# Optimization experiments

Hardware: AMD Instinct MI355X
Metric: run time of the kernel (lower is better)

The kernel has to match this reference:

```python
import jax, jax.numpy as jnp
import numpy as np

B, S, D = 4, 2048, 1024
H = 16            # n_heads
HD = D // H       # head_dim = 64
F = 64            # feature_dim of linear-attention feature map


def setup_inputs() -> dict:
    key = jax.random.key(0)
    ks = jax.random.split(key, 16)
    w = lambda k, shape: jax.random.normal(k, shape, dtype=jnp.float32) * 0.02
    return {
        "x": jax.random.normal(ks[0], (B, S, D), dtype=jnp.float32),
        # flash-attention branch params (Linear stored as [in, out])
        "fq": w(ks[1], (D, D)),
        "fk": w(ks[2], (D, D)),
        "fv": w(ks[3], (D, D)),
        "fo_w": w(ks[4], (D, D)),
        "fo_b": jnp.zeros((D,), jnp.float32),
        # linear-attention branch params
        "lq": w(ks[5], (D, D)),
        "lk": w(ks[6], (D, D)),
        "lv": w(ks[7], (D, D)),
        "lo_w": w(ks[8], (D, D)),
        "lo_b": jnp.zeros((D,), jnp.float32),
        "fm_w": w(ks[9], (HD, F)),
        "fm_b": jnp.zeros((F,), jnp.float32),
        # gate
        "gate_w": w(ks[10], (D, 1)),
        "gate_b": jnp.zeros((1,), jnp.float32),
    }


def reference(x, fq, fk, fv, fo_w, fo_b, lq, lk, lv, lo_w, lo_b,
              fm_w, fm_b, gate_w, gate_b):
    b, s, d = x.shape
    # ---- flash (standard softmax) attention path ----
    q = (x @ fq).reshape(b, s, H, HD)
    k = (x @ fk).reshape(b, s, H, HD)
    v = (x @ fv).reshape(b, s, H, HD)
    scale = 1.0 / np.sqrt(HD).astype(np.float32)
    scores = jnp.einsum('bqhd,bkhd->bhqk', q, k) * scale
    attn = jax.nn.softmax(scores, axis=-1)
    flash = jnp.einsum('bhqk,bkhd->bqhd', attn, v).reshape(b, s, d)
    flash_out = flash @ fo_w + fo_b
    # ---- linear (kernelized) attention path ----
    ql = (x @ lq).reshape(b, s, H, HD)
    kl = (x @ lk).reshape(b, s, H, HD)
    vl = (x @ lv).reshape(b, s, H, HD)
    qf = jax.nn.relu(ql @ fm_w + fm_b)   # [b,s,h,f]
    kf = jax.nn.relu(kl @ fm_w + fm_b)
    kv = jnp.einsum('blhf,blhd->bhfd', kf, vl)
    lin = jnp.einsum('blhf,bhfd->blhd', qf, kv)
    k_sum = kf.sum(axis=1)                               # [b,h,f]
    norm = jnp.einsum('blhf,bhf->blh', qf, k_sum)[..., None]
    lin = lin / jnp.maximum(norm, 1e-6)
    linear_out = lin.reshape(b, s, d) @ lo_w + lo_b
    # ---- sigmoid gate blend ----
    gate = jax.nn.sigmoid(x @ gate_w + gate_b)           # [b,s,1]
    return gate * flash_out + (1.0 - gate) * linear_out
```

## Files before the change

kernel.cpp:

```cpp
#include <hip/hip_runtime.h>
#include <math.h>

typedef __attribute__((ext_vector_type(4))) float f32x4;
typedef __attribute__((ext_vector_type(16))) float f32x16;
typedef __attribute__((ext_vector_type(8))) short s16x8;
typedef __attribute__((ext_vector_type(8))) unsigned short u16x8;

constexpr int Bc = 4, Sc = 2048, Dc = 1024, Hc = 16, HDc = 64, Fc = 64;
constexpr int Rc = Bc * Sc;
constexpr size_t MAT = (size_t)Rc * Dc;
constexpr int KST = 88;
constexpr int NCH = 16;

__device__ __forceinline__ float bf2f(unsigned short u) {
    union { unsigned int i; float f; } v; v.i = ((unsigned int)u) << 16; return v.f;
}
__device__ __forceinline__ unsigned short f2bf(float f) {
    union { float f; unsigned int i; } v; v.f = f;
    unsigned int r = v.i + 0x7FFFu + ((v.i >> 16) & 1u);
    return (unsigned short)(r >> 16);
}
__device__ __forceinline__ unsigned cvtpk(float a, float b) {
    unsigned r;
    asm("v_cvt_pk_bf16_f32 %0, %1, %2" : "=v"(r) : "v"(a), "v"(b));
    return r;
}
__device__ __forceinline__ void async16(const void* g, void* l) {
    __builtin_amdgcn_global_load_lds(
        (const __attribute__((address_space(1))) unsigned int*)g,
        (__attribute__((address_space(3))) unsigned int*)l, 16, 0, 0);
}

__global__ __launch_bounds__(256) void gate_cvt(const float* __restrict__ x,
        const float* __restrict__ gw, const float* __restrict__ gb,
        float* __restrict__ G, unsigned short* __restrict__ Y) {
    const int lane = threadIdx.x & 63;
    const int wave = threadIdx.x >> 6;
    const int r = blockIdx.x * 4 + wave;
    const size_t base = (size_t)r * Dc;
    float acc = 0.f;
    #pragma unroll
    for (int i = 0; i < 4; ++i) {
        int off = (lane + 64 * i) * 4;
        float4 v = *(const float4*)(x + base + off);
        float4 w = *(const float4*)(gw + off);
        acc += v.x * w.x + v.y * w.y + v.z * w.z + v.w * w.w;
        ushort4 o;
        o.x = f2bf(v.x); o.y = f2bf(v.y); o.z = f2bf(v.z); o.w = f2bf(v.w);
        *(ushort4*)(Y + base + off) = o;
    }
    #pragma unroll
    for (int off = 32; off > 0; off >>= 1) acc += __shfl_down(acc, off, 64);
    if (lane == 0) {
        float z = acc + gb[0];
        G[r] = 1.f / (1.f + __expf(-z));
    }
}

__global__ __launch_bounds__(256) void wtrans(
        const float* W0, const float* W1, const float* W2, const float* W3,
        const float* W4, const float* W5, const float* W6, const float* W7,
        unsigned short* T0, unsigned short* T1, unsigned short* T2, unsigned short* T3,
        unsigned short* T4, unsigned short* T5, unsigned short* T6, unsigned short* T7) {
    const float* W; unsigned short* T;
    switch (blockIdx.z) {
        case 0: W = W0; T = T0; break;  case 1: W = W1; T = T1; break;
        case 2: W = W2; T = T2; break;  case 3: W = W3; T = T3; break;
        case 4: W = W4; T = T4; break;  case 5: W = W5; T = T5; break;
        case 6: W = W6; T = T6; break;  default: W = W7; T = T7; break;
    }
    __shared__ float tile[64][65];
    const int t = threadIdx.x;
    const int r0 = blockIdx.x * 64, c0 = blockIdx.y * 64;
    #pragma unroll
    for (int i = 0; i < 4; ++i) {
        int row = (t >> 4) + 16 * i, col = (t & 15) * 4;
        float4 v = *(const float4*)(W + (size_t)(r0 + row) * 1024 + c0 + col);
        tile[row][col] = v.x; tile[row][col + 1] = v.y;
        tile[row][col + 2] = v.z; tile[row][col + 3] = v.w;
    }
    __syncthreads();
    #pragma unroll
    for (int i = 0; i < 4; ++i) {
        int orow = (t >> 4) + 16 * i, ocol = (t & 15) * 4;
        ushort4 o;
        o.x = f2bf(tile[ocol][orow]);     o.y = f2bf(tile[ocol + 1][orow]);
        o.z = f2bf(tile[ocol + 2][orow]); o.w = f2bf(tile[ocol + 3][orow]);
        *(ushort4*)(T + (size_t)(c0 + orow) * 1024 + r0 + ocol) = o;
    }
}

__global__ __launch_bounds__(256) void gemm3(const unsigned short* __restrict__ A,
        const unsigned short* __restrict__ WT, unsigned short* __restrict__ C0,
        unsigned short* __restrict__ C1, unsigned short* __restrict__ C2) {
    __shared__ unsigned short As[128 * 32];
    __shared__ unsigned short Bs[128 * 32];
    const int tid = threadIdx.x, wave = tid >> 6, lane = tid & 63;
    const int brow = blockIdx.x * 128;
    const int bcolg = blockIdx.y * 128;
    unsigned short* C = (blockIdx.y < 8) ? C0 : (blockIdx.y < 16 ? C1 : C2);
    const int bcol = bcolg & 1023;
    const int wm = wave >> 1, wn = wave & 1;
    const int lr = lane & 15, g8 = (lane >> 4) * 8;
    const int srow = 32 * wave + (lane >> 2);
    const int scol = (lane & 3) * 8;
    f32x4 acc[4][4];
    #pragma unroll
    for (int m = 0; m < 4; ++m)
        #pragma unroll
        for (int n = 0; n < 4; ++n) acc[m][n] = (f32x4){0.f, 0.f, 0.f, 0.f};
    for (int k0 = 0; k0 < 1024; k0 += 32) {
        __syncthreads();
        #pragma unroll
        for (int i = 0; i < 2; ++i) {
            async16(A  + (size_t)(brow  + srow + 16 * i) * 1024 + k0 + scol, &As[(32 * wave + 16 * i) * 32]);
            async16(WT + (size_t)(bcolg + srow + 16 * i) * 1024 + k0 + scol, &Bs[(32 * wave + 16 * i) * 32]);
        }
        __syncthreads();
        s16x8 af[4], bf[4];
        #pragma unroll
        for (int m = 0; m < 4; ++m) af[m] = *(const s16x8*)&As[(64 * wm + 16 * m + lr) * 32 + g8];
        #pragma unroll
        for (int n = 0; n < 4; ++n) bf[n] = *(const s16x8*)&Bs[(64 * wn + 16 * n + lr) * 32 + g8];
        #pragma unroll
        for (int m = 0; m < 4; ++m)
            #pragma unroll
            for (int n = 0; n < 4; ++n)
                acc[m][n] = __builtin_amdgcn_mfma_f32_16x16x32_bf16(af[m], bf[n], acc[m][n], 0, 0, 0);
    }
    const int rg = (lane >> 4) * 4;
    #pragma unroll
    for (int m = 0; m < 4; ++m)
        #pragma unroll
        for (int n = 0; n < 4; ++n)
            #pragma unroll
            for (int j = 0; j < 4; ++j)
                C[(size_t)(brow + 64 * wm + 16 * m + rg + j) * 1024 + bcol + 64 * wn + 16 * n + lr] =
                    f2bf(acc[m][n][j]);
}

__global__ __launch_bounds__(256) void final_gemm(const unsigned short* __restrict__ A1,
        const unsigned short* __restrict__ WT1, const unsigned short* __restrict__ A2,
        const unsigned short* __restrict__ WT2, const float* __restrict__ b1,
        const float* __restrict__ b2, const float* __restrict__ G, float* __restrict__ OUT) {
    __shared__ unsigned short As[128 * 32];
    __shared__ unsigned short Bs[128 * 32];
    const int tid = threadIdx.x, wave = tid >> 6, lane = tid & 63;
    const int brow = blockIdx.x * 128, bcol = blockIdx.y * 128;
    const int wm = wave >> 1, wn = wave & 1;
    const int lr = lane & 15, g8 = (lane >> 4) * 8;
    const int srow = 32 * wave + (lane >> 2);
    const int scol = (lane & 3) * 8;
    f32x4 acc[4][4];
    #pragma unroll
    for (int m = 0; m < 4; ++m)
        #pragma unroll
        for (int n = 0; n < 4; ++n) acc[m][n] = (f32x4){0.f, 0.f, 0.f, 0.f};
    for (int pass = 0; pass < 2; ++pass) {
        const unsigned short* A  = pass ? A2 : A1;
        const unsigned short* WT = pass ? WT2 : WT1;
        for (int k0 = 0; k0 < 1024; k0 += 32) {
            __syncthreads();
            #pragma unroll
            for (int i = 0; i < 2; ++i) {
                async16(A  + (size_t)(brow + srow + 16 * i) * 1024 + k0 + scol, &As[(32 * wave + 16 * i) * 32]);
                async16(WT + (size_t)(bcol + srow + 16 * i) * 1024 + k0 + scol, &Bs[(32 * wave + 16 * i) * 32]);
            }
            __syncthreads();
            s16x8 af[4], bf[4];
            #pragma unroll
            for (int m = 0; m < 4; ++m) af[m] = *(const s16x8*)&As[(64 * wm + 16 * m + lr) * 32 + g8];
            #pragma unroll
            for (int n = 0; n < 4; ++n) bf[n] = *(const s16x8*)&Bs[(64 * wn + 16 * n + lr) * 32 + g8];
            #pragma unroll
            for (int m = 0; m < 4; ++m)
                #pragma unroll
                for (int n = 0; n < 4; ++n)
                    acc[m][n] = __builtin_amdgcn_mfma_f32_16x16x32_bf16(af[m], bf[n], acc[m][n], 0, 0, 0);
        }
    }
    const int rg = (lane >> 4) * 4;
    #pragma unroll
    for (int m = 0; m < 4; ++m)
        #pragma unroll
        for (int j = 0; j < 4; ++j) {
            int row = brow + 64 * wm + 16 * m + rg + j;
            float g = G[row];
            #pragma unroll
            for (int n = 0; n < 4; ++n) {
                int col = bcol + 64 * wn + 16 * n + lr;
                OUT[(size_t)row * 1024 + col] = acc[m][n][j] + g * b1[col] + (1.f - g) * b2[col];
            }
        }
}

__global__ __launch_bounds__(256) void flash_mfma(const unsigned short* __restrict__ Qg,
        const unsigned short* __restrict__ Kg, const unsigned short* __restrict__ Vg,
        const float* __restrict__ G, unsigned short* __restrict__ FA) {
    __shared__ unsigned short Ks[2][64 * KST];
    __shared__ unsigned short Vt[2][64 * KST];
    const int tid = threadIdx.x, wave = tid >> 6, lane = tid & 63;
    const int b = blockIdx.z, h = blockIdx.y, q0 = blockIdx.x * 128;
    const int lq = lane & 31, hi = lane >> 5;
    const float QSCALE = 0.125f * 1.44269504f;
    const size_t qrow = (size_t)b * Sc + q0 + wave * 32 + lq;
    const size_t qoff = qrow * Dc + h * HDc + 8 * hi;
    s16x8 aq[4];
    #pragma unroll
    for (int dc = 0; dc < 4; ++dc) {
        u16x8 raw = *(const u16x8*)(Qg + qoff + 16 * dc);
        #pragma unroll
        for (int j = 0; j < 8; ++j) aq[dc][j] = (short)f2bf(bf2f(raw[j]) * QSCALE);
    }
    f32x16 oacc[2];
    #pragma unroll
    for (int t = 0; t < 2; ++t)
        #pragma unroll
        for (int r = 0; r < 16; ++r) oacc[t][r] = 0.f;
    float l_run = 0.f;
    const int srow = tid >> 3, sc8 = (tid & 7) * 8, va = tid & 7;
    const int p0 = (srow & 3) | (((srow >> 3) & 1) << 2) | (((srow >> 2) & 1) << 3) | (srow & 0x10);
    const int pg = p0 >> 3, pin = p0 & 7;
    const size_t kvoff = (size_t)h * HDc + sc8;
    #pragma unroll
    for (int r = 0; r < 2; ++r) {
        int row = srow + 32 * r;
        size_t gg = ((size_t)b * Sc + row) * Dc + kvoff;
        u16x8 kreg = *(const u16x8*)(Kg + gg);
        u16x8 vreg = *(const u16x8*)(Vg + gg);
        *(u16x8*)&Ks[0][row * KST + sc8] = kreg;
        #pragma unroll
        for (int j = 0; j < 8; ++j)
            Vt[0][(sc8 + j) * KST + 8 * ((pg + 4 * r) ^ va) + pin] = vreg[j];
    }
    __syncthreads();
    int cur = 0;
    for (int t0 = 0; t0 < Sc; t0 += 64) {
        const bool nxt = (t0 + 64) < Sc;
        u16x8 kn0, kn1, vn0, vn1;
        if (nxt) {
            size_t gg0 = ((size_t)b * Sc + t0 + 64 + srow) * Dc + kvoff;
            kn0 = *(const u16x8*)(Kg + gg0);
            vn0 = *(const u16x8*)(Vg + gg0);
            size_t gg1 = gg0 + (size_t)32 * Dc;
            kn1 = *(const u16x8*)(Kg + gg1);
            vn1 = *(const u16x8*)(Vg + gg1);
        }
        f32x16 s2[2];
        #pragma unroll
        for (int t = 0; t < 2; ++t)
            #pragma unroll
            for (int r = 0; r < 16; ++r) s2[t][r] = 0.f;
        __builtin_amdgcn_s_setprio(1);
        #pragma unroll
        for (int kt2 = 0; kt2 < 2; ++kt2)
            #pragma unroll
            for (int dc = 0; dc < 4; ++dc) {
                s16x8 ak = *(const s16x8*)&Ks[cur][(32 * kt2 + lq) * KST + 16 * dc + 8 * hi];
                s2[kt2] = __builtin_amdgcn_mfma_f32_32x32x16_bf16(ak, aq[dc], s2[kt2], 0, 0, 0);
            }
        __builtin_amdgcn_s_setprio(0);
        float ls[4] = {0.f, 0.f, 0.f, 0.f};
        #pragma unroll
        for (int t = 0; t < 2; ++t)
            #pragma unroll
            for (int r = 0; r < 16; ++r) {
                s2[t][r] = exp2f(s2[t][r]);
                ls[r & 3] += s2[t][r];
            }
        float lsum = (ls[0] + ls[1]) + (ls[2] + ls[3]);
        lsum += __shfl_xor(lsum, 32, 64);
        l_run += lsum;
        s16x8 pf[4];
        #pragma unroll
        for (int kc = 0; kc < 4; ++kc) {
            const int t = kc >> 1, e = 8 * (kc & 1);
            union { s16x8 v; unsigned u[4]; } w;
            w.u[0] = cvtpk(s2[t][e + 0], s2[t][e + 1]);
            w.u[1] = cvtpk(s2[t][e + 2], s2[t][e + 3]);
            w.u[2] = cvtpk(s2[t][e + 4], s2[t][e + 5]);
            w.u[3] = cvtpk(s2[t][e + 6], s2[t][e + 7]);
            pf[kc] = w.v;
        }
        __builtin_amdgcn_s_setprio(1);
        #pragma unroll
        for (int dtile = 0; dtile < 2; ++dtile) {
            const int row = 32 * dtile + lq;
            const int rsw = (row >> 3) & 7;
            #pragma unroll
            for (int kc = 0; kc < 4; ++kc) {
                const int g = 4 * (kc >> 1) + 2 * (kc & 1) + hi;
                s16x8 av = *(const s16x8*)&Vt[cur][row * KST + 8 * (g ^ rsw)];
                oacc[dtile] = __builtin_amdgcn_mfma_f32_32x32x16_bf16(av, pf[kc], oacc[dtile], 0, 0, 0);
            }
        }
        __builtin_amdgcn_s_setprio(0);
        if (nxt) {
            *(u16x8*)&Ks[cur ^ 1][srow * KST + sc8] = kn0;
            *(u16x8*)&Ks[cur ^ 1][(srow + 32) * KST + sc8] = kn1;
            #pragma unroll
            for (int j = 0; j < 8; ++j) {
                Vt[cur ^ 1][(sc8 + j) * KST + 8 * (pg ^ va) + pin] = vn0[j];
                Vt[cur ^ 1][(sc8 + j) * KST + 8 * ((pg + 4) ^ va) + pin] = vn1[j];
            }
        }
        __syncthreads();
        cur ^= 1;
    }
    const float scl = G[qrow] / l_run;
    #pragma unroll
    for (int dtile = 0; dtile < 2; ++dtile)
        #pragma unroll
        for (int s = 0; s < 4; ++s) {
            ushort4 o4;
            o4.x = f2bf(oacc[dtile][4 * s + 0] * scl);
            o4.y = f2bf(oacc[dtile][4 * s + 1] * scl);
            o4.z = f2bf(oacc[dtile][4 * s + 2] * scl);
            o4.w = f2bf(oacc[dtile][4 * s + 3] * scl);
            *(ushort4*)(FA + qrow * Dc + h * HDc + 32 * dtile + 8 * s + 4 * hi) = o4;
        }
}

__global__ __launch_bounds__(256) void featmap_kernel(unsigned short* __restrict__ QL,
        unsigned short* __restrict__ KL, const float* __restrict__ fmw, const float* __restrict__ fmb) {
    __shared__ float Wf[64][68];
    __shared__ float bs[64];
    __shared__ float Xs[16][68];
    const int tid = threadIdx.x;
    for (int i = tid; i < 64 * 64 / 4; i += 256) {
        int r = i >> 4, c = (i & 15) << 2;
        *(float4*)&Wf[r][c] = *(const float4*)(fmw + r * 64 + c);
    }
    if (tid < 64) bs[tid] = fmb[tid];
    const size_t row0 = (size_t)blockIdx.x * 16;
    const int rr = tid >> 4;
    const int fg = (tid & 15) << 2;
    for (int pass = 0; pass < 2; ++pass) {
        unsigned short* X = pass ? KL : QL;
        __syncthreads();
        {
            int r = tid >> 4, c = (tid & 15) << 2;
            ushort4 xv = *(const ushort4*)(X + (row0 + r) * 64 + c);
            Xs[r][c] = bf2f(xv.x); Xs[r][c + 1] = bf2f(xv.y);
            Xs[r][c + 2] = bf2f(xv.z); Xs[r][c + 3] = bf2f(xv.w);
        }
        __syncthreads();
        float a0 = bs[fg], a1 = bs[fg + 1], a2 = bs[fg + 2], a3 = bs[fg + 3];
        #pragma unroll 8
        for (int d = 0; d < 64; ++d) {
            float xv = Xs[rr][d];
            float4 w = *(const float4*)&Wf[d][fg];
            a0 += xv * w.x; a1 += xv * w.y; a2 += xv * w.z; a3 += xv * w.w;
        }
        ushort4 ov;
        ov.x = f2bf(fmaxf(a0, 0.f)); ov.y = f2bf(fmaxf(a1, 0.f));
        ov.z = f2bf(fmaxf(a2, 0.f)); ov.w = f2bf(fmaxf(a3, 0.f));
        *(ushort4*)(X + (row0 + rr) * 64 + fg) = ov;
    }
}

__global__ __launch_bounds__(256) void kv_part(const unsigned short* __restrict__ KF,
        const unsigned short* __restrict__ VL, float* __restrict__ PART, float* __restrict__ PARTS) {
    __shared__ float Ks[32][68];
    __shared__ float Vs[32][68];
    const int tid = threadIdx.x;
    const int bh = blockIdx.x;
    const int b = bh >> 4, h = bh & 15;
    const int ch = blockIdx.y;
    const int f = tid >> 2;
    const int dg = (tid & 3) << 4;
    float acc[16] = {};
    float ksum = 0.f;
    const int lbeg = ch * (Sc / NCH), lend = lbeg + Sc / NCH;
    for (int l0 = lbeg; l0 < lend; l0 += 32) {
        __syncthreads();
        for (int i = tid; i < 32 * 64 / 4; i += 256) {
            int r = i >> 4, c = (i & 15) << 2;
            size_t gg = ((size_t)(b * Sc + l0 + r) * Hc + h) * 64 + c;
            ushort4 kk = *(const ushort4*)(KF + gg);
            ushort4 vv = *(const ushort4*)(VL + gg);
            Ks[r][c] = bf2f(kk.x); Ks[r][c + 1] = bf2f(kk.y);
            Ks[r][c + 2] = bf2f(kk.z); Ks[r][c + 3] = bf2f(kk.w);
            Vs[r][c] = bf2f(vv.x); Vs[r][c + 1] = bf2f(vv.y);
            Vs[r][c + 2] = bf2f(vv.z); Vs[r][c + 3] = bf2f(vv.w);
        }
        __syncthreads();
        #pragma unroll 4
        for (int ll = 0; ll < 32; ++ll) {
            float kf = Ks[ll][f];
            ksum += kf;
            float4 v0 = *(const float4*)&Vs[ll][dg];
            float4 v1 = *(const float4*)&Vs[ll][dg + 4];
            float4 v2 = *(const float4*)&Vs[ll][dg + 8];
            float4 v3 = *(const float4*)&Vs[ll][dg + 12];
            acc[0] += kf * v0.x; acc[1] += kf * v0.y; acc[2]  += kf * v0.z; acc[3]  += kf * v0.w;
            acc[4] += kf * v1.x; acc[5] += kf * v1.y; acc[6]  += kf * v1.z; acc[7]  += kf * v1.w;
            acc[8] += kf * v2.x; acc[9] += kf * v2.y; acc[10] += kf * v2.z; acc[11] += kf * v2.w;
            acc[12] += kf * v3.x; acc[13] += kf * v3.y; acc[14] += kf * v3.z; acc[15] += kf * v3.w;
        }
    }
    size_t o = (((size_t)ch * 64 + bh) * 64 + f) * 64 + dg;
    *(float4*)(PART + o)      = make_float4(acc[0], acc[1], acc[2], acc[3]);
    *(float4*)(PART + o + 4)  = make_float4(acc[4], acc[5], acc[6], acc[7]);
    *(float4*)(PART + o + 8)  = make_float4(acc[8], acc[9], acc[10], acc[11]);
    *(float4*)(PART + o + 12) = make_float4(acc[12], acc[13], acc[14], acc[15]);
    if ((tid & 3) == 0) PARTS[((size_t)ch * 64 + bh) * 64 + f] = ksum;
}

__global__ __launch_bounds__(256) void kv_reduce(const float* __restrict__ PART,
        float* __restrict__ KV) {
    size_t i = (size_t)blockIdx.x * 256 + threadIdx.x;
    float s = 0.f;
    #pragma unroll
    for (int ch = 0; ch < NCH; ++ch) s += PART[(size_t)ch * 262144 + i];
    KV[i] = s;
}
__global__ __launch_bounds__(256) void ks_reduce(const float* __restrict__ PARTS,
        float* __restrict__ KS) {
    int i = blockIdx.x * 256 + threadIdx.x;
    float s = 0.f;
    #pragma unroll
    for (int ch = 0; ch < NCH; ++ch) s += PARTS[ch * 4096 + i];
    KS[i] = s;
}

__global__ __launch_bounds__(256) void lin_kernel(const unsigned short* __restrict__ QF,
        const float* __restrict__ KV, const float* __restrict__ KSUM,
        const float* __restrict__ G, unsigned short* __restrict__ LA) {
    __shared__ float Qs[4][68];
    __shared__ float Ss[4][68];
    const int tid = threadIdx.x;
    const size_t i0 = (size_t)blockIdx.x * 4;
    {
        int r = tid >> 6, c = tid & 63;
        size_t i = i0 + r;
        int bh = (int)(i / ((size_t)Sc * Hc)) * Hc + (int)(i & (Hc - 1));
        Qs[r][c] = bf2f(QF[i * 64 + c]);
        Ss[r][c] = KSUM[(size_t)bh * 64 + c];
    }
    __syncthreads();
    const int r = tid >> 6, d = tid & 63;
    const size_t i = i0 + r;
    const int bh = (int)(i / ((size_t)Sc * Hc)) * Hc + (int)(i & (Hc - 1));
    const float* kvp = KV + (size_t)bh * 64 * 64 + d;
    float acc = 0.f, nrm = 0.f;
    #pragma unroll 8
    for (int ff = 0; ff < 64; ++ff) {
        float q = Qs[r][ff];
        acc += q * kvp[(size_t)ff * 64];
        nrm += q * Ss[r][ff];
    }
    float g = G[(int)(i >> 4)];
    LA[i * 64 + d] = f2bf((1.f - g) * acc / fmaxf(nrm, 1e-6f));
}

extern "C" void kernel_launch(void* const* d_in, const int* in_sizes, int n_in,
                              void* d_out, int out_size, void* d_ws, size_t ws_size,
                              hipStream_t stream) {
    const float* x   = (const float*)d_in[0];
    const float* fq  = (const float*)d_in[1];
    const float* fk  = (const float*)d_in[2];
    const float* fv  = (const float*)d_in[3];
    const float* fow = (const float*)d_in[4];
    const float* fob = (const float*)d_in[5];
    const float* lq  = (const float*)d_in[6];
    const float* lk  = (const float*)d_in[7];
    const float* lv  = (const float*)d_in[8];
    const float* low = (const float*)d_in[9];
    const float* lob = (const float*)d_in[10];
    const float* fmw = (const float*)d_in[11];
    const float* fmb = (const float*)d_in[12];
    const float* gw  = (const float*)d_in[13];
    const float* gb  = (const float*)d_in[14];
    float* out = (float*)d_out;

    char* p = (char*)d_ws;
    unsigned short* xb = (unsigned short*)p;          p += MAT * 2;
    unsigned short* wt_fq = (unsigned short*)p;       p += (size_t)1024 * 1024 * 2;
    unsigned short* wt_fk = (unsigned short*)p;       p += (size_t)1024 * 1024 * 2;
    unsigned short* wt_fv = (unsigned short*)p;       p += (size_t)1024 * 1024 * 2;
    unsigned short* wt_fo = (unsigned short*)p;       p += (size_t)1024 * 1024 * 2;
    unsigned short* wt_lq = (unsigned short*)p;       p += (size_t)1024 * 1024 * 2;
    unsigned short* wt_lk = (unsigned short*)p;       p += (size_t)1024 * 1024 * 2;
    unsigned short* wt_lv = (unsigned short*)p;       p += (size_t)1024 * 1024 * 2;
    unsigned short* wt_lo = (unsigned short*)p;       p += (size_t)1024 * 1024 * 2;
    unsigned short* P0 = (unsigned short*)p;          p += MAT * 2;
    unsigned short* P1 = (unsigned short*)p;          p += MAT * 2;
    unsigned short* P2 = (unsigned short*)p;          p += MAT * 2;
    unsigned short* FA = (unsigned short*)p;          p += MAT * 2;
    unsigned short* LA = (unsigned short*)p;          p += MAT * 2;
    float* KV = (float*)p;                            p += (size_t)Bc * Hc * Fc * HDc * 4;
    float* KS = (float*)p;                            p += (size_t)Bc * Hc * Fc * 4;
    float* G  = (float*)p;                            p += (size_t)Rc * 4;
    float* PART  = (float*)p;                         p += (size_t)NCH * 64 * 64 * 64 * 4;
    float* PARTS = (float*)p;                         p += (size_t)NCH * 64 * 64 * 4;

    dim3 proj3Grid(Rc / 128, 24);
    dim3 gemmGrid(Rc / 128, Dc / 128);

    gate_cvt<<<Rc / 4, 256, 0, stream>>>(x, gw, gb, G, xb);
    wtrans<<<dim3(16, 16, 8), 256, 0, stream>>>(fq, fk, fv, fow, lq, lk, lv, low,
            wt_fq, wt_fk, wt_fv, wt_fo, wt_lq, wt_lk, wt_lv, wt_lo);

    gemm3<<<proj3Grid, 256, 0, stream>>>(xb, wt_lq, P0, P1, P2);
    featmap_kernel<<<Rc * Hc / 16, 256, 0, stream>>>(P0, P1, fmw, fmb);
    kv_part<<<dim3(Bc * Hc, NCH), 256, 0, stream>>>(P1, P2, PART, PARTS);
    kv_reduce<<<(64 * 64 * 64) / 256, 256, 0, stream>>>(PART, KV);
    ks_reduce<<<(64 * 64) / 256, 256, 0, stream>>>(PARTS, KS);
    lin_kernel<<<Rc * Hc / 4, 256, 0, stream>>>(P0, KV, KS, G, LA);

    gemm3<<<proj3Grid, 256, 0, stream>>>(xb, wt_fq, P0, P1, P2);
    flash_mfma<<<dim3(Sc / 128, Hc, Bc), 256, 0, stream>>>(P0, P1, P2, G, FA);

    final_gemm<<<gemmGrid, 256, 0, stream>>>(FA, wt_fo, LA, wt_lo, fob, lob, G, out);
}
```

Measured before the change: 459.4 us.

## Double flash block to 8 waves and compute row sums via MFMA with ones

The flash attention kernel now runs 512 threads per block, covering 256 query rows, so each K/V tile staged in shared memory is reused by twice as many waves. Each thread loads one K/V row per tile instead of two. The softmax denominator is no longer summed with VALU adds and a cross-lane shuffle; it comes from an extra MFMA that multiplies the probability fragments by a ones vector. The extra MFMA work per tile and the bf16-rounded probabilities feeding the denominator trade some precision and matrix throughput for less VALU work. Halving the block count may also reduce occupancy balance across CUs.

```diff
diff --git a/kernel.cpp b/kernel.cpp
--- a/kernel.cpp
+++ b/kernel.cpp
@@ -194,13 +194,13 @@
         }
 }
 
-__global__ __launch_bounds__(256) void flash_mfma(const unsigned short* __restrict__ Qg,
+__global__ __launch_bounds__(512) void flash_mfma(const unsigned short* __restrict__ Qg,
         const unsigned short* __restrict__ Kg, const unsigned short* __restrict__ Vg,
         const float* __restrict__ G, unsigned short* __restrict__ FA) {
     __shared__ unsigned short Ks[2][64 * KST];
     __shared__ unsigned short Vt[2][64 * KST];
     const int tid = threadIdx.x, wave = tid >> 6, lane = tid & 63;
-    const int b = blockIdx.z, h = blockIdx.y, q0 = blockIdx.x * 128;
+    const int b = blockIdx.z, h = blockIdx.y, q0 = blockIdx.x * 256;
     const int lq = lane & 31, hi = lane >> 5;
     const float QSCALE = 0.125f * 1.44269504f;
     const size_t qrow = (size_t)b * Sc + q0 + wave * 32 + lq;
@@ -212,39 +212,36 @@
         #pragma unroll
         for (int j = 0; j < 8; ++j) aq[dc][j] = (short)f2bf(bf2f(raw[j]) * QSCALE);
     }
-    f32x16 oacc[2];
+    const s16x8 ones = {0x3F80, 0x3F80, 0x3F80, 0x3F80, 0x3F80, 0x3F80, 0x3F80, 0x3F80};
+    f32x16 oacc[2], lacc;
     #pragma unroll
     for (int t = 0; t < 2; ++t)
         #pragma unroll
         for (int r = 0; r < 16; ++r) oacc[t][r] = 0.f;
-    float l_run = 0.f;
+    #pragma unroll
+    for (int r = 0; r < 16; ++r) lacc[r] = 0.f;
     const int srow = tid >> 3, sc8 = (tid & 7) * 8, va = tid & 7;
-    const int p0 = (srow & 3) | (((srow >> 3) & 1) << 2) | (((srow >> 2) & 1) << 3) | (srow & 0x10);
+    const int p0 = (srow & 3) | (((srow >> 3) & 1) << 2) | (((srow >> 2) & 1) << 3) | (srow & 0x30);
     const int pg = p0 >> 3, pin = p0 & 7;
     const size_t kvoff = (size_t)h * HDc + sc8;
-    #pragma unroll
-    for (int r = 0; r < 2; ++r) {
-        int row = srow + 32 * r;
-        size_t gg = ((size_t)b * Sc + row) * Dc + kvoff;
+    {
+        size_t gg = ((size_t)b * Sc + srow) * Dc + kvoff;
         u16x8 kreg = *(const u16x8*)(Kg + gg);
         u16x8 vreg = *(const u16x8*)(Vg + gg);
-        *(u16x8*)&Ks[0][row * KST + sc8] = kreg;
+        *(u16x8*)&Ks[0][srow * KST + sc8] = kreg;
         #pragma unroll
         for (int j = 0; j < 8; ++j)
-            Vt[0][(sc8 + j) * KST + 8 * ((pg + 4 * r) ^ va) + pin] = vreg[j];
+            Vt[0][(sc8 + j) * KST + 8 * (pg ^ va) + pin] = vreg[j];
     }
     __syncthreads();
     int cur = 0;
     for (int t0 = 0; t0 < Sc; t0 += 64) {
         const bool nxt = (t0 + 64) < Sc;
-        u16x8 kn0, kn1, vn0, vn1;
+        u16x8 kn, vn;
         if (nxt) {
-            size_t gg0 = ((size_t)b * Sc + t0 + 64 + srow) * Dc + kvoff;
-            kn0 = *(const u16x8*)(Kg + gg0);
-            vn0 = *(const u16x8*)(Vg + gg0);
-            size_t gg1 = gg0 + (size_t)32 * Dc;
-            kn1 = *(const u16x8*)(Kg + gg1);
-            vn1 = *(const u16x8*)(Vg + gg1);
+            size_t gg = ((size_t)b * Sc + t0 + 64 + srow) * Dc + kvoff;
+            kn = *(const u16x8*)(Kg + gg);
+            vn = *(const u16x8*)(Vg + gg);
         }
         f32x16 s2[2];
         #pragma unroll
@@ -260,17 +257,11 @@
                 s2[kt2] = __builtin_amdgcn_mfma_f32_32x32x16_bf16(ak, aq[dc], s2[kt2], 0, 0, 0);
             }
         __builtin_amdgcn_s_setprio(0);
-        float ls[4] = {0.f, 0.f, 0.f, 0.f};
         #pragma unroll
         for (int t = 0; t < 2; ++t)
             #pragma unroll
-            for (int r = 0; r < 16; ++r) {
+            for (int r = 0; r < 16; ++r)
                 s2[t][r] = exp2f(s2[t][r]);
-                ls[r & 3] += s2[t][r];
-            }
-        float lsum = (ls[0] + ls[1]) + (ls[2] + ls[3]);
-        lsum += __shfl_xor(lsum, 32, 64);
-        l_run += lsum;
         s16x8 pf[4];
         #pragma unroll
         for (int kc = 0; kc < 4; ++kc) {
@@ -294,20 +285,20 @@
                 oacc[dtile] = __builtin_amdgcn_mfma_f32_32x32x16_bf16(av, pf[kc], oacc[dtile], 0, 0, 0);
             }
         }
+        #pragma unroll
+        for (int kc = 0; kc < 4; ++kc)
+            lacc = __builtin_amdgcn_mfma_f32_32x32x16_bf16(ones, pf[kc], lacc, 0, 0, 0);
         __builtin_amdgcn_s_setprio(0);
         if (nxt) {
-            *(u16x8*)&Ks[cur ^ 1][srow * KST + sc8] = kn0;
-            *(u16x8*)&Ks[cur ^ 1][(srow + 32) * KST + sc8] = kn1;
-            #pragma unroll
-            for (int j = 0; j < 8; ++j) {
-                Vt[cur ^ 1][(sc8 + j) * KST + 8 * (pg ^ va) + pin] = vn0[j];
-                Vt[cur ^ 1][(sc8 + j) * KST + 8 * ((pg + 4) ^ va) + pin] = vn1[j];
-            }
+            *(u16x8*)&Ks[cur ^ 1][srow * KST + sc8] = kn;
+            #pragma unroll
+            for (int j = 0; j < 8; ++j)
+                Vt[cur ^ 1][(sc8 + j) * KST + 8 * (pg ^ va) + pin] = vn[j];
         }
         __syncthreads();
         cur ^= 1;
     }
-    const float scl = G[qrow] / l_run;
+    const float scl = G[qrow] / lacc[0];
     #pragma unroll
     for (int dtile = 0; dtile < 2; ++dtile)
         #pragma unroll
@@ -510,7 +501,7 @@
     lin_kernel<<<Rc * Hc / 4, 256, 0, stream>>>(P0, KV, KS, G, LA);
 
     gemm3<<<proj3Grid, 256, 0, stream>>>(xb, wt_fq, P0, P1, P2);
-    flash_mfma<<<dim3(Sc / 128, Hc, Bc), 256, 0, stream>>>(P0, P1, P2, G, FA);
+    flash_mfma<<<dim3(Sc / 256, Hc, Bc), 512, 0, stream>>>(P0, P1, P2, G, FA);
 
     final_gemm<<<gemmGrid, 256, 0, stream>>>(FA, wt_fo, LA, wt_lo, fob, lob, G, out);
 }
```

Result: no change. 455.8 us (-0.8%).
